# Performance work log

Hardware: AMD Instinct MI355X
Metric: run time of the kernel (lower is better)

## Reference

```python
import jax, jax.numpy as jnp
import numpy as np

N = 50000      # nodes
E = 800000     # edges (avg degree 16)
D = 128        # d_model
H = 8          # num_heads
DK = D // H    # d_k = 16


def setup_inputs() -> dict:
    key = jax.random.key(0)
    ks = jax.random.split(key, 9)
    scale = np.float32(1.0 / np.sqrt(D))
    return {
        "q": jax.random.normal(ks[0], (N, D), jnp.float32),
        "k": jax.random.normal(ks[1], (N, D), jnp.float32),
        "v": jax.random.normal(ks[2], (N, D), jnp.float32),
        "e": jax.random.normal(ks[3], (E, D), jnp.float32),
        "src": jax.random.randint(ks[4], (E,), 0, N),
        "dst": jax.random.randint(ks[5], (E,), 0, N),
        # nn.Linear(D, D, bias=False) weights, stored as [in, out]
        "Wq": jax.random.normal(ks[6], (D, D), jnp.float32) * scale,
        "Wk": jax.random.normal(ks[7], (D, D), jnp.float32) * scale,
        "Wv": jax.random.normal(ks[8], (D, D), jnp.float32) * scale,
    }


def reference(q, k, v, e, src, dst, Wq, Wk, Wv):
    inv_sqrt_dk = np.float32(1.0 / np.sqrt(DK))
    # node-level V projection, then per-edge gather of src V  -> [E, H, DK]
    Vn = (v @ Wv).reshape(N, H, DK)
    Ve = Vn[src]
    # per-edge Q from dst node, K from (src k + edge feature e)
    Qe = (q[dst] @ Wq).reshape(E, H, DK)
    Ke = ((k[src] + e) @ Wk).reshape(E, H, DK)
    # per-edge HxH score matrix: Q @ K^T / sqrt(d_k), leaky-relu
    s = jnp.einsum("ehd,egd->ehg", Qe, Ke) * inv_sqrt_dk   # [E, H, H]
    s = jax.nn.leaky_relu(s)
    # softmax over last head axis (within each edge, as in reduce_func dim=-1)
    A = jax.nn.softmax(s, axis=-1)
    # per-edge message, heads regrouped -> [E, D]
    He = jnp.einsum("ehg,egd->ehd", A, Ve).reshape(E, D)
    # plain sum over incoming edges per destination node -> [N, D]
    return jax.ops.segment_sum(He, dst, num_segments=N)
```

## Files before the change

kernel.cpp:

```cpp
#include <hip/hip_runtime.h>
#include <hip/hip_bf16.h>
#include <math.h>

#define NN 50000
#define EE 800000
#define DD 128
#define HH 8
#define DKK 16

typedef __attribute__((ext_vector_type(8))) short short8;
typedef __attribute__((ext_vector_type(4))) float f32x4;
typedef __attribute__((ext_vector_type(4))) unsigned short ushort4v;
typedef __attribute__((ext_vector_type(8))) unsigned short ushort8v;

static __device__ __forceinline__ unsigned short f2bf(float x) {
  __hip_bfloat16 h = __float2bfloat16(x);
  return *reinterpret_cast<unsigned short*>(&h);
}
static __device__ __forceinline__ float bf2f(unsigned short u) {
  return __uint_as_float(((unsigned int)u) << 16);
}

__global__ __launch_bounds__(256) void hist_kernel(const int* __restrict__ dst,
                                                   int* __restrict__ cnt) {
  int i4 = blockIdx.x * 256 + threadIdx.x;
  if (i4 < EE / 4) {
    int4 d = *(const int4*)&dst[i4 * 4];
    atomicAdd(&cnt[d.x], 1);
    atomicAdd(&cnt[d.y], 1);
    atomicAdd(&cnt[d.z], 1);
    atomicAdd(&cnt[d.w], 1);
  }
}

#define SCAN_NB ((NN + 1023) / 1024)

__global__ __launch_bounds__(256) void scan1_kernel(const int* __restrict__ cnt,
                                                    int* __restrict__ bsum) {
  __shared__ int red[256];
  const int b = blockIdx.x, t = threadIdx.x;
  const int base = b * 1024 + t * 4;
  int s = 0;
  if (base + 3 < NN) {
    int4 v = *(const int4*)&cnt[base];
    s = v.x + v.y + v.z + v.w;
  } else {
    for (int j = 0; j < 4; ++j) if (base + j < NN) s += cnt[base + j];
  }
  red[t] = s;
  __syncthreads();
  for (int off = 1; off < 256; off <<= 1) {
    int v = (t >= off) ? red[t - off] : 0;
    __syncthreads();
    red[t] += v;
    __syncthreads();
  }
  if (t == 255) bsum[b] = red[255];
}

__global__ __launch_bounds__(64) void scan2_kernel(const int* __restrict__ bsum,
                                                   int* __restrict__ bpre) {
  int t = threadIdx.x;
  int v = (t < SCAN_NB) ? bsum[t] : 0;
  for (int off = 1; off < 64; off <<= 1) {
    int u = __shfl_up(v, off);
    if (t >= off) v += u;
  }
  if (t < SCAN_NB) bpre[t + 1] = v;
  if (t == 0) bpre[0] = 0;
}

__global__ __launch_bounds__(256) void scan3_kernel(const int* __restrict__ cnt,
                                                    const int* __restrict__ bpre,
                                                    int* __restrict__ rowptr) {
  __shared__ int red[256];
  const int b = blockIdx.x, t = threadIdx.x;
  const int base = b * 1024 + t * 4;
  int v0 = 0, v1 = 0, v2 = 0, v3 = 0;
  if (base + 3 < NN) {
    int4 v = *(const int4*)&cnt[base];
    v0 = v.x; v1 = v.y; v2 = v.z; v3 = v.w;
  } else {
    if (base + 0 < NN) v0 = cnt[base + 0];
    if (base + 1 < NN) v1 = cnt[base + 1];
    if (base + 2 < NN) v2 = cnt[base + 2];
    if (base + 3 < NN) v3 = cnt[base + 3];
  }
  red[t] = v0 + v1 + v2 + v3;
  __syncthreads();
  for (int off = 1; off < 256; off <<= 1) {
    int v = (t >= off) ? red[t - off] : 0;
    __syncthreads();
    red[t] += v;
    __syncthreads();
  }
  int r = bpre[b] + ((t == 0) ? 0 : red[t - 1]);
  if (base + 0 < NN) { rowptr[base + 0] = r; r += v0; }
  if (base + 1 < NN) { rowptr[base + 1] = r; r += v1; }
  if (base + 2 < NN) { rowptr[base + 2] = r; r += v2; }
  if (base + 3 < NN) { rowptr[base + 3] = r; }
}

__global__ __launch_bounds__(256) void fill_kernel(const int* __restrict__ dst,
                                                   const int* __restrict__ rowptr,
                                                   int* __restrict__ cur,
                                                   int* __restrict__ perm) {
  int i4 = blockIdx.x * 256 + threadIdx.x;
  if (i4 < EE / 4) {
    int4 dv = *(const int4*)&dst[i4 * 4];
    int d0 = dv.x, d1 = dv.y, d2 = dv.z, d3 = dv.w;
    int s0 = atomicAdd(&cur[d0], 1); perm[rowptr[d0] + s0] = i4 * 4 + 0;
    int s1 = atomicAdd(&cur[d1], 1); perm[rowptr[d1] + s1] = i4 * 4 + 1;
    int s2 = atomicAdd(&cur[d2], 1); perm[rowptr[d2] + s2] = i4 * 4 + 2;
    int s3 = atomicAdd(&cur[d3], 1); perm[rowptr[d3] + s3] = i4 * 4 + 3;
  }
}

__global__ void prep_w_kernel(const float* __restrict__ Wq,
                              const float* __restrict__ Wk,
                              const float* __restrict__ Wv,
                              unsigned short* __restrict__ WqT,
                              unsigned short* __restrict__ WkT,
                              unsigned short* __restrict__ WvT) {
  int c = blockIdx.x & 127;
  int m = blockIdx.x >> 7;
  int j = threadIdx.x;
  const float* W = (m == 0) ? Wq : (m == 1) ? Wk : Wv;
  unsigned short* o = (m == 0) ? WqT : (m == 1) ? WkT : WvT;
  o[j * DD + c] = f2bf(W[c * DD + j]);
}

__global__ __launch_bounds__(512) void node_proj_kernel(
    const float* __restrict__ q, const float* __restrict__ v,
    const float* __restrict__ k,
    const unsigned short* __restrict__ WqT, const unsigned short* __restrict__ WvT,
    unsigned short* __restrict__ Qh, unsigned short* __restrict__ Vh,
    unsigned short* __restrict__ kh)
{
  __shared__ __align__(16) unsigned short xl[64 * 136];
  const int tid = threadIdx.x;
  const int n0 = blockIdx.x * 64;

  #pragma unroll
  for (int p = 0; p < 2; ++p) {
    int f = p * 512 + tid;
    int i = f >> 4, c8 = f & 15;
    int n = n0 + i;
    if (n < NN) {
      float4 a = *(const float4*)&k[(size_t)n * DD + c8 * 8];
      float4 b = *(const float4*)&k[(size_t)n * DD + c8 * 8 + 4];
      ushort8v o = { f2bf(a.x), f2bf(a.y), f2bf(a.z), f2bf(a.w),
                     f2bf(b.x), f2bf(b.y), f2bf(b.z), f2bf(b.w) };
      *(ushort8v*)&kh[(size_t)n * DD + c8 * 8] = o;
    }
  }

  for (int m = 0; m < 2; ++m) {
    const float* x = m ? v : q;
    const unsigned short* WT = m ? WvT : WqT;
    unsigned short* o = m ? Vh : Qh;

    __syncthreads();
    #pragma unroll
    for (int p = 0; p < 4; ++p) {
      int f = p * 512 + tid;
      int i = f >> 5, c4 = f & 31;
      int n = n0 + i;
      float4 t = (n < NN) ? *(const float4*)&x[(size_t)n * DD + c4 * 4]
                          : float4{0.f, 0.f, 0.f, 0.f};
      ushort4v u = { f2bf(t.x), f2bf(t.y), f2bf(t.z), f2bf(t.w) };
      *(ushort4v*)&xl[i * 136 + c4 * 4] = u;
    }
    __syncthreads();

    const int lane = tid & 63, wid = tid >> 6;
    const int rg = wid & 3, cg = wid >> 2;
    const int lr = lane & 15, lg = lane >> 4;

    f32x4 acc0 = {0.f,0.f,0.f,0.f}, acc1 = {0.f,0.f,0.f,0.f};
    f32x4 acc2 = {0.f,0.f,0.f,0.f}, acc3 = {0.f,0.f,0.f,0.f};

    const unsigned short* Ab = &xl[(rg * 16 + lr) * 136];
    const unsigned short* B0 = &WT[(size_t)(cg * 64 +  0 + lr) * DD];
    const unsigned short* B1 = &WT[(size_t)(cg * 64 + 16 + lr) * DD];
    const unsigned short* B2 = &WT[(size_t)(cg * 64 + 32 + lr) * DD];
    const unsigned short* B3 = &WT[(size_t)(cg * 64 + 48 + lr) * DD];

    #pragma unroll
    for (int kk = 0; kk < 4; ++kk) {
      const int kof = kk * 32 + lg * 8;
      short8 a = *(const short8*)(Ab + kof);
      acc0 = __builtin_amdgcn_mfma_f32_16x16x32_bf16(a, *(const short8*)(B0 + kof), acc0, 0, 0, 0);
      acc1 = __builtin_amdgcn_mfma_f32_16x16x32_bf16(a, *(const short8*)(B1 + kof), acc1, 0, 0, 0);
      acc2 = __builtin_amdgcn_mfma_f32_16x16x32_bf16(a, *(const short8*)(B2 + kof), acc2, 0, 0, 0);
      acc3 = __builtin_amdgcn_mfma_f32_16x16x32_bf16(a, *(const short8*)(B3 + kof), acc3, 0, 0, 0);
    }

    const int r0 = rg * 16 + lg * 4;
    const int cb = cg * 64 + lr;
    #pragma unroll
    for (int r = 0; r < 4; ++r) {
      int n = n0 + r0 + r;
      if (n < NN) {
        unsigned short* orow = &o[(size_t)n * DD + cb];
        orow[ 0] = f2bf(acc0[r]);
        orow[16] = f2bf(acc1[r]);
        orow[32] = f2bf(acc2[r]);
        orow[48] = f2bf(acc3[r]);
      }
    }
  }
}

__global__ __launch_bounds__(512) void edge_attn_kernel(
    const unsigned short* __restrict__ kh, const float* __restrict__ e,
    const int* __restrict__ src, const int* __restrict__ dst,
    const int* __restrict__ perm,
    const unsigned short* __restrict__ WkT,
    const unsigned short* __restrict__ Qh, const unsigned short* __restrict__ Vh,
    float* __restrict__ out)
{
  __shared__ __align__(16) unsigned short buf[128 * 136];
  __shared__ __align__(16) unsigned short vbuf[128 * 136];
  __shared__ int s_perm[128], s_src[128], s_dst[128];

  const int tid = threadIdx.x;
  const size_t e0 = (size_t)blockIdx.x * 128;

  if (tid < 128) {
    int pe = perm[e0 + tid];
    s_perm[tid] = pe;
    s_src[tid] = src[pe];
    s_dst[tid] = dst[pe];
  }
  __syncthreads();

  #pragma unroll
  for (int p = 0; p < 4; ++p) {
    int f = p * 512 + tid;
    int i2 = f >> 4, c8 = f & 15;
    *(ushort8v*)&vbuf[i2 * 136 + c8 * 8] =
        *(const ushort8v*)&Vh[(size_t)s_src[i2] * DD + c8 * 8];
  }

  const int i0 = tid >> 3, i1 = i0 + 64, h = tid & 7;
  const int dn0 = s_dst[i0], dn1 = s_dst[i1];
  ushort8v qa0 = *(const ushort8v*)&Qh[(size_t)dn0 * DD + h * DKK];
  ushort8v qa1 = *(const ushort8v*)&Qh[(size_t)dn0 * DD + h * DKK + 8];
  ushort8v qb0 = *(const ushort8v*)&Qh[(size_t)dn1 * DD + h * DKK];
  ushort8v qb1 = *(const ushort8v*)&Qh[(size_t)dn1 * DD + h * DKK + 8];

  #pragma unroll
  for (int p = 0; p < 4; ++p) {
    int f = p * 512 + tid;
    int i2 = f >> 4, c8 = f & 15;
    ushort8v kv = *(const ushort8v*)&kh[(size_t)s_src[i2] * DD + c8 * 8];
    float4 ea = *(const float4*)&e[(size_t)s_perm[i2] * DD + c8 * 8];
    float4 eb = *(const float4*)&e[(size_t)s_perm[i2] * DD + c8 * 8 + 4];
    ushort8v o;
    o[0] = f2bf(bf2f(kv[0]) + ea.x);
    o[1] = f2bf(bf2f(kv[1]) + ea.y);
    o[2] = f2bf(bf2f(kv[2]) + ea.z);
    o[3] = f2bf(bf2f(kv[3]) + ea.w);
    o[4] = f2bf(bf2f(kv[4]) + eb.x);
    o[5] = f2bf(bf2f(kv[5]) + eb.y);
    o[6] = f2bf(bf2f(kv[6]) + eb.z);
    o[7] = f2bf(bf2f(kv[7]) + eb.w);
    *(ushort8v*)&buf[i2 * 136 + c8 * 8] = o;
  }
  __syncthreads();

  {
    const int lane = tid & 63, wid = tid >> 6;
    const int rgA = wid & 3, rgB = (wid & 3) + 4, cg = wid >> 2;
    const int lr = lane & 15, lg = lane >> 4;

    f32x4 aA0 = {0.f,0.f,0.f,0.f}, aA1 = {0.f,0.f,0.f,0.f};
    f32x4 aA2 = {0.f,0.f,0.f,0.f}, aA3 = {0.f,0.f,0.f,0.f};
    f32x4 aB0 = {0.f,0.f,0.f,0.f}, aB1 = {0.f,0.f,0.f,0.f};
    f32x4 aB2 = {0.f,0.f,0.f,0.f}, aB3 = {0.f,0.f,0.f,0.f};

    const unsigned short* AbA = &buf[(rgA * 16 + lr) * 136];
    const unsigned short* AbB = &buf[(rgB * 16 + lr) * 136];
    const unsigned short* B0 = &WkT[(size_t)(cg * 64 +  0 + lr) * DD];
    const unsigned short* B1 = &WkT[(size_t)(cg * 64 + 16 + lr) * DD];
    const unsigned short* B2 = &WkT[(size_t)(cg * 64 + 32 + lr) * DD];
    const unsigned short* B3 = &WkT[(size_t)(cg * 64 + 48 + lr) * DD];

    #pragma unroll
    for (int kk = 0; kk < 4; ++kk) {
      const int kof = kk * 32 + lg * 8;
      short8 b0 = *(const short8*)(B0 + kof);
      short8 b1 = *(const short8*)(B1 + kof);
      short8 b2 = *(const short8*)(B2 + kof);
      short8 b3 = *(const short8*)(B3 + kof);
      short8 fA = *(const short8*)(AbA + kof);
      short8 fB = *(const short8*)(AbB + kof);
      aA0 = __builtin_amdgcn_mfma_f32_16x16x32_bf16(fA, b0, aA0, 0, 0, 0);
      aA1 = __builtin_amdgcn_mfma_f32_16x16x32_bf16(fA, b1, aA1, 0, 0, 0);
      aA2 = __builtin_amdgcn_mfma_f32_16x16x32_bf16(fA, b2, aA2, 0, 0, 0);
      aA3 = __builtin_amdgcn_mfma_f32_16x16x32_bf16(fA, b3, aA3, 0, 0, 0);
      aB0 = __builtin_amdgcn_mfma_f32_16x16x32_bf16(fB, b0, aB0, 0, 0, 0);
      aB1 = __builtin_amdgcn_mfma_f32_16x16x32_bf16(fB, b1, aB1, 0, 0, 0);
      aB2 = __builtin_amdgcn_mfma_f32_16x16x32_bf16(fB, b2, aB2, 0, 0, 0);
      aB3 = __builtin_amdgcn_mfma_f32_16x16x32_bf16(fB, b3, aB3, 0, 0, 0);
    }

    __syncthreads();

    const int rA = rgA * 16 + lg * 4;
    const int rB = rgB * 16 + lg * 4;
    const int cb = cg * 64 + lr;
    #pragma unroll
    for (int r = 0; r < 4; ++r) {
      buf[(rA + r) * 136 + cb +  0] = f2bf(aA0[r]);
      buf[(rA + r) * 136 + cb + 16] = f2bf(aA1[r]);
      buf[(rA + r) * 136 + cb + 32] = f2bf(aA2[r]);
      buf[(rA + r) * 136 + cb + 48] = f2bf(aA3[r]);
      buf[(rB + r) * 136 + cb +  0] = f2bf(aB0[r]);
      buf[(rB + r) * 136 + cb + 16] = f2bf(aB1[r]);
      buf[(rB + r) * 136 + cb + 32] = f2bf(aB2[r]);
      buf[(rB + r) * 136 + cb + 48] = f2bf(aB3[r]);
    }
  }
  __syncthreads();

  float sc0[8], sc1[8];
  {
    #pragma unroll
    for (int g = 0; g < 8; ++g) {
      const ushort8v* kp = (const ushort8v*)&buf[i0 * 136 + g * DKK];
      ushort8v k0 = kp[0], k1 = kp[1];
      float a = 0.0f;
      #pragma unroll
      for (int t = 0; t < 8; ++t) a = fmaf(bf2f(qa0[t]), bf2f(k0[t]), a);
      #pragma unroll
      for (int t = 0; t < 8; ++t) a = fmaf(bf2f(qa1[t]), bf2f(k1[t]), a);
      a *= 0.25f;
      sc0[g] = (a >= 0.0f) ? a : 0.01f * a;
    }
    #pragma unroll
    for (int g = 0; g < 8; ++g) {
      const ushort8v* kp = (const ushort8v*)&buf[i1 * 136 + g * DKK];
      ushort8v k0 = kp[0], k1 = kp[1];
      float a = 0.0f;
      #pragma unroll
      for (int t = 0; t < 8; ++t) a = fmaf(bf2f(qb0[t]), bf2f(k0[t]), a);
      #pragma unroll
      for (int t = 0; t < 8; ++t) a = fmaf(bf2f(qb1[t]), bf2f(k1[t]), a);
      a *= 0.25f;
      sc1[g] = (a >= 0.0f) ? a : 0.01f * a;
    }
    float mx0 = sc0[0], mx1 = sc1[0];
    #pragma unroll
    for (int g = 1; g < 8; ++g) { mx0 = fmaxf(mx0, sc0[g]); mx1 = fmaxf(mx1, sc1[g]); }
    float su0 = 0.0f, su1 = 0.0f;
    #pragma unroll
    for (int g = 0; g < 8; ++g) {
      sc0[g] = __expf(sc0[g] - mx0); su0 += sc0[g];
      sc1[g] = __expf(sc1[g] - mx1); su1 += sc1[g];
    }
    float r0 = 1.0f / su0, r1 = 1.0f / su1;
    #pragma unroll
    for (int g = 0; g < 8; ++g) { sc0[g] *= r0; sc1[g] *= r1; }
  }
  __syncthreads();

  {
    float he[16];
    #pragma unroll
    for (int d = 0; d < 16; ++d) he[d] = 0.0f;
    #pragma unroll
    for (int g = 0; g < 8; ++g) {
      float a = sc0[g];
      const ushort8v* vp = (const ushort8v*)&vbuf[i0 * 136 + g * DKK];
      ushort8v v0 = vp[0], v1 = vp[1];
      #pragma unroll
      for (int t = 0; t < 8; ++t) {
        he[t]     = fmaf(a, bf2f(v0[t]), he[t]);
        he[8 + t] = fmaf(a, bf2f(v1[t]), he[8 + t]);
      }
    }
    ushort8v o0, o1;
    #pragma unroll
    for (int t = 0; t < 8; ++t) { o0[t] = f2bf(he[t]); o1[t] = f2bf(he[8 + t]); }
    *(ushort8v*)&buf[i0 * 136 + h * DKK]     = o0;
    *(ushort8v*)&buf[i0 * 136 + h * DKK + 8] = o1;

    #pragma unroll
    for (int d = 0; d < 16; ++d) he[d] = 0.0f;
    #pragma unroll
    for (int g = 0; g < 8; ++g) {
      float a = sc1[g];
      const ushort8v* vp = (const ushort8v*)&vbuf[i1 * 136 + g * DKK];
      ushort8v v0 = vp[0], v1 = vp[1];
      #pragma unroll
      for (int t = 0; t < 8; ++t) {
        he[t]     = fmaf(a, bf2f(v0[t]), he[t]);
        he[8 + t] = fmaf(a, bf2f(v1[t]), he[8 + t]);
      }
    }
    #pragma unroll
    for (int t = 0; t < 8; ++t) { o0[t] = f2bf(he[t]); o1[t] = f2bf(he[8 + t]); }
    *(ushort8v*)&buf[i1 * 136 + h * DKK]     = o0;
    *(ushort8v*)&buf[i1 * 136 + h * DKK + 8] = o1;
  }
  __syncthreads();

  {
    const int c = tid >> 6, d2 = tid & 63;
    const int base = c * 16;
    float s0 = 0.0f, s1 = 0.0f;
    int curd = s_dst[base];
    #pragma unroll 8
    for (int j = 0; j < 16; ++j) {
      int i2 = base + j;
      int dn2 = s_dst[i2];
      if (dn2 != curd) {
        atomicAdd(&out[(size_t)curd * DD + d2 * 2],     s0);
        atomicAdd(&out[(size_t)curd * DD + d2 * 2 + 1], s1);
        s0 = 0.0f; s1 = 0.0f;
        curd = dn2;
      }
      unsigned int w = *(const unsigned int*)&buf[i2 * 136 + d2 * 2];
      s0 += bf2f((unsigned short)(w & 0xffff));
      s1 += bf2f((unsigned short)(w >> 16));
    }
    atomicAdd(&out[(size_t)curd * DD + d2 * 2],     s0);
    atomicAdd(&out[(size_t)curd * DD + d2 * 2 + 1], s1);
  }
}

extern "C" void kernel_launch(void* const* d_in, const int* in_sizes, int n_in,
                              void* d_out, int out_size, void* d_ws, size_t ws_size,
                              hipStream_t stream) {
  const float* q  = (const float*)d_in[0];
  const float* k  = (const float*)d_in[1];
  const float* v  = (const float*)d_in[2];
  const float* e  = (const float*)d_in[3];
  const int*   src = (const int*)d_in[4];
  const int*   dst = (const int*)d_in[5];
  const float* Wq = (const float*)d_in[6];
  const float* Wk = (const float*)d_in[7];
  const float* Wv = (const float*)d_in[8];

  float* out = (float*)d_out;
  char* wsb = (char*)d_ws;
  unsigned short* Qh  = (unsigned short*)wsb;
  unsigned short* Vh  = Qh + (size_t)NN * DD;
  unsigned short* kh  = Vh + (size_t)NN * DD;
  unsigned short* WqT = kh + (size_t)NN * DD;
  unsigned short* WkT = WqT + DD * DD;
  unsigned short* WvT = WkT + DD * DD;
  int* cnt    = (int*)(WvT + DD * DD);
  int* cur    = cnt + NN;
  int* rowptr = cur + NN;
  int* bsum   = rowptr + NN + 1;
  int* bpre   = bsum + 64;
  int* perm   = bpre + 64;

  hipMemsetAsync(d_out, 0, (size_t)NN * DD * sizeof(float), stream);
  hipMemsetAsync(cnt, 0, 2 * NN * sizeof(int), stream);

  hist_kernel <<<(EE / 4 + 255) / 256, 256, 0, stream>>>(dst, cnt);
  scan1_kernel<<<SCAN_NB, 256, 0, stream>>>(cnt, bsum);
  scan2_kernel<<<1, 64, 0, stream>>>(bsum, bpre);
  scan3_kernel<<<SCAN_NB, 256, 0, stream>>>(cnt, bpre, rowptr);
  fill_kernel <<<(EE / 4 + 255) / 256, 256, 0, stream>>>(dst, rowptr, cur, perm);

  prep_w_kernel<<<3 * DD, DD, 0, stream>>>(Wq, Wk, Wv, WqT, WkT, WvT);
  node_proj_kernel<<<(NN + 63) / 64, 512, 0, stream>>>(q, v, k, WqT, WvT,
                                                       Qh, Vh, kh);
  edge_attn_kernel<<<EE / 128, 512, 0, stream>>>(kh, e, src, dst, perm,
                                                 WkT, Qh, Vh, out);
}
```

Before: 378.5 us.

## Compute per-edge head scores and attention-value products with MFMA instead of scalar FMAs

Replaces the scalar per-thread HxH score and A·V loops with bf16 16x16x32 MFMA instructions. Each wave handles two edges per step by packing them into a block-diagonal 16x16 tile, with off-diagonal scores masked to a large negative value. Softmax runs across lanes via shuffles, and probabilities are staged through a small per-wave shared buffer. It drops the scalar FMA work and one block-wide barrier, but half of each MFMA is wasted on padding and the V operand uses strided scalar LDS reads.

After: 387.3 us. 1.02x slower.

```diff
diff --git a/kernel.cpp b/kernel.cpp
--- a/kernel.cpp
+++ b/kernel.cpp
@@ -222,6 +222,7 @@
 {
   __shared__ __align__(16) unsigned short buf[128 * 136];
   __shared__ __align__(16) unsigned short vbuf[128 * 136];
+  __shared__ __align__(16) unsigned short pbuf[8 * 16 * 24];
   __shared__ int s_perm[128], s_src[128], s_dst[128];
 
   const int tid = threadIdx.x;
@@ -242,13 +243,6 @@
     *(ushort8v*)&vbuf[i2 * 136 + c8 * 8] =
         *(const ushort8v*)&Vh[(size_t)s_src[i2] * DD + c8 * 8];
   }
-
-  const int i0 = tid >> 3, i1 = i0 + 64, h = tid & 7;
-  const int dn0 = s_dst[i0], dn1 = s_dst[i1];
-  ushort8v qa0 = *(const ushort8v*)&Qh[(size_t)dn0 * DD + h * DKK];
-  ushort8v qa1 = *(const ushort8v*)&Qh[(size_t)dn0 * DD + h * DKK + 8];
-  ushort8v qb0 = *(const ushort8v*)&Qh[(size_t)dn1 * DD + h * DKK];
-  ushort8v qb1 = *(const ushort8v*)&Qh[(size_t)dn1 * DD + h * DKK + 8];
 
   #pragma unroll
   for (int p = 0; p < 4; ++p) {
@@ -270,10 +264,11 @@
   }
   __syncthreads();
 
+  const int lane = tid & 63, wid = tid >> 6;
+  const int lr = lane & 15, lg = lane >> 4;
+
   {
-    const int lane = tid & 63, wid = tid >> 6;
     const int rgA = wid & 3, rgB = (wid & 3) + 4, cg = wid >> 2;
-    const int lr = lane & 15, lg = lane >> 4;
 
     f32x4 aA0 = {0.f,0.f,0.f,0.f}, aA1 = {0.f,0.f,0.f,0.f};
     f32x4 aA2 = {0.f,0.f,0.f,0.f}, aA3 = {0.f,0.f,0.f,0.f};
@@ -325,87 +320,84 @@
   }
   __syncthreads();
 
-  float sc0[8], sc1[8];
   {
-    #pragma unroll
-    for (int g = 0; g < 8; ++g) {
-      const ushort8v* kp = (const ushort8v*)&buf[i0 * 136 + g * DKK];
-      ushort8v k0 = kp[0], k1 = kp[1];
-      float a = 0.0f;
+    const int ebase = wid * 16;
+    const bool valid = ((lr < 8) == (lg < 2));
+    unsigned short* pb = &pbuf[wid * 16 * 24];
+    const short8 zero8 = {0, 0, 0, 0, 0, 0, 0, 0};
+
+    short8 qf[8];
+    #pragma unroll
+    for (int j = 0; j < 8; ++j) {
+      if (lg < 2) {
+        int ie = ebase + 2 * j + (lr >> 3);
+        qf[j] = *(const short8*)&Qh[(size_t)s_dst[ie] * DD + (lr & 7) * DKK + lg * 8];
+      } else qf[j] = zero8;
+    }
+
+    #pragma unroll
+    for (int j = 0; j < 8; ++j) {
+      const int iea = ebase + 2 * j, ieb = iea + 1;
+
+      short8 af = zero8;
+      if (lg < 2) {
+        int ie = (lr < 8) ? iea : ieb;
+        af = *(const short8*)&buf[ie * 136 + (lr & 7) * DKK + lg * 8];
+      }
+      f32x4 c = {0.f, 0.f, 0.f, 0.f};
+      c = __builtin_amdgcn_mfma_f32_16x16x32_bf16(af, qf[j], c, 0, 0, 0);
+
+      float s0, s1, s2, s3;
+      {
+        float x0 = c[0] * 0.25f, x1 = c[1] * 0.25f;
+        float x2 = c[2] * 0.25f, x3 = c[3] * 0.25f;
+        x0 = (x0 >= 0.f) ? x0 : 0.01f * x0;
+        x1 = (x1 >= 0.f) ? x1 : 0.01f * x1;
+        x2 = (x2 >= 0.f) ? x2 : 0.01f * x2;
+        x3 = (x3 >= 0.f) ? x3 : 0.01f * x3;
+        s0 = valid ? x0 : -1e30f;
+        s1 = valid ? x1 : -1e30f;
+        s2 = valid ? x2 : -1e30f;
+        s3 = valid ? x3 : -1e30f;
+      }
+      float m = fmaxf(fmaxf(s0, s1), fmaxf(s2, s3));
+      m = fmaxf(m, __shfl_xor(m, 16));
+      m = fmaxf(m, __shfl_xor(m, 32));
+      float p0 = __expf(s0 - m), p1 = __expf(s1 - m);
+      float p2 = __expf(s2 - m), p3 = __expf(s3 - m);
+      float su = p0 + p1 + p2 + p3;
+      su += __shfl_xor(su, 16);
+      su += __shfl_xor(su, 32);
+      float rs = 1.0f / su;
+
+      ushort4v pk = { f2bf(p0 * rs), f2bf(p1 * rs), f2bf(p2 * rs), f2bf(p3 * rs) };
+      *(ushort4v*)&pb[lr * 24 + lg * 4] = pk;
+
+      short8 pa = zero8;
+      if (lg < 2) pa = *(const short8*)&pb[lr * 24 + lg * 8];
+      short8 vf = zero8;
+      if (lg < 2) {
+        const unsigned short* vr = &vbuf[(lg ? ieb : iea) * 136 + lr];
+        vf[0] = (short)vr[0 * 16];
+        vf[1] = (short)vr[1 * 16];
+        vf[2] = (short)vr[2 * 16];
+        vf[3] = (short)vr[3 * 16];
+        vf[4] = (short)vr[4 * 16];
+        vf[5] = (short)vr[5 * 16];
+        vf[6] = (short)vr[6 * 16];
+        vf[7] = (short)vr[7 * 16];
+      }
+      f32x4 hc = {0.f, 0.f, 0.f, 0.f};
+      hc = __builtin_amdgcn_mfma_f32_16x16x32_bf16(pa, vf, hc, 0, 0, 0);
+
       #pragma unroll
-      for (int t = 0; t < 8; ++t) a = fmaf(bf2f(qa0[t]), bf2f(k0[t]), a);
-      #pragma unroll
-      for (int t = 0; t < 8; ++t) a = fmaf(bf2f(qa1[t]), bf2f(k1[t]), a);
-      a *= 0.25f;
-      sc0[g] = (a >= 0.0f) ? a : 0.01f * a;
-    }
-    #pragma unroll
-    for (int g = 0; g < 8; ++g) {
-      const ushort8v* kp = (const ushort8v*)&buf[i1 * 136 + g * DKK];
-      ushort8v k0 = kp[0], k1 = kp[1];
-      float a = 0.0f;
-      #pragma unroll
-      for (int t = 0; t < 8; ++t) a = fmaf(bf2f(qb0[t]), bf2f(k0[t]), a);
-      #pragma unroll
-      for (int t = 0; t < 8; ++t) a = fmaf(bf2f(qb1[t]), bf2f(k1[t]), a);
-      a *= 0.25f;
-      sc1[g] = (a >= 0.0f) ? a : 0.01f * a;
-    }
-    float mx0 = sc0[0], mx1 = sc1[0];
-    #pragma unroll
-    for (int g = 1; g < 8; ++g) { mx0 = fmaxf(mx0, sc0[g]); mx1 = fmaxf(mx1, sc1[g]); }
-    float su0 = 0.0f, su1 = 0.0f;
-    #pragma unroll
-    for (int g = 0; g < 8; ++g) {
-      sc0[g] = __expf(sc0[g] - mx0); su0 += sc0[g];
-      sc1[g] = __expf(sc1[g] - mx1); su1 += sc1[g];
-    }
-    float r0 = 1.0f / su0, r1 = 1.0f / su1;
-    #pragma unroll
-    for (int g = 0; g < 8; ++g) { sc0[g] *= r0; sc1[g] *= r1; }
-  }
-  __syncthreads();
-
-  {
-    float he[16];
-    #pragma unroll
-    for (int d = 0; d < 16; ++d) he[d] = 0.0f;
-    #pragma unroll
-    for (int g = 0; g < 8; ++g) {
-      float a = sc0[g];
-      const ushort8v* vp = (const ushort8v*)&vbuf[i0 * 136 + g * DKK];
-      ushort8v v0 = vp[0], v1 = vp[1];
-      #pragma unroll
-      for (int t = 0; t < 8; ++t) {
-        he[t]     = fmaf(a, bf2f(v0[t]), he[t]);
-        he[8 + t] = fmaf(a, bf2f(v1[t]), he[8 + t]);
-      }
-    }
-    ushort8v o0, o1;
-    #pragma unroll
-    for (int t = 0; t < 8; ++t) { o0[t] = f2bf(he[t]); o1[t] = f2bf(he[8 + t]); }
-    *(ushort8v*)&buf[i0 * 136 + h * DKK]     = o0;
-    *(ushort8v*)&buf[i0 * 136 + h * DKK + 8] = o1;
-
-    #pragma unroll
-    for (int d = 0; d < 16; ++d) he[d] = 0.0f;
-    #pragma unroll
-    for (int g = 0; g < 8; ++g) {
-      float a = sc1[g];
-      const ushort8v* vp = (const ushort8v*)&vbuf[i1 * 136 + g * DKK];
-      ushort8v v0 = vp[0], v1 = vp[1];
-      #pragma unroll
-      for (int t = 0; t < 8; ++t) {
-        he[t]     = fmaf(a, bf2f(v0[t]), he[t]);
-        he[8 + t] = fmaf(a, bf2f(v1[t]), he[8 + t]);
-      }
-    }
-    #pragma unroll
-    for (int t = 0; t < 8; ++t) { o0[t] = f2bf(he[t]); o1[t] = f2bf(he[8 + t]); }
-    *(ushort8v*)&buf[i1 * 136 + h * DKK]     = o0;
-    *(ushort8v*)&buf[i1 * 136 + h * DKK + 8] = o1;
-  }
-  __syncthreads();
+      for (int r = 0; r < 4; ++r) {
+        int rr = lg * 4 + r;
+        int ie = (rr < 8) ? iea : ieb;
+        buf[ie * 136 + (rr & 7) * DKK + lr] = f2bf(hc[r]);
+      }
+    }
+  }
 
   {
     const int c = tid >> 6, d2 = tid & 63;
```
